# Kernel optimization log

Measured on AMD Instinct MI355X. Metric: run time of the kernel, lower is better.

Reference implementation:

```python
import jax, jax.numpy as jnp
import numpy as np

D_MODEL = 1024
N_HEADS = 16
D_HEAD = 64


def setup_inputs() -> dict:
    key = jax.random.key(0)
    kx, kq, kk, kv, ko = jax.random.split(key, 5)
    B, T = 2, 2048
    inner = N_HEADS * D_HEAD
    s = 1.0 / np.sqrt(D_MODEL)
    return {
        "x": jax.random.normal(kx, (B, T, D_MODEL), dtype=jnp.float32),
        "Wq": jax.random.normal(kq, (D_MODEL, inner), dtype=jnp.float32) * s,
        "Wk": jax.random.normal(kk, (D_MODEL, inner), dtype=jnp.float32) * s,
        "Wv": jax.random.normal(kv, (D_MODEL, inner), dtype=jnp.float32) * s,
        "Wo": jax.random.normal(ko, (inner, D_MODEL), dtype=jnp.float32) * (1.0 / np.sqrt(inner)),
    }


def reference(x, Wq, Wk, Wv, Wo):
    B, T, D = x.shape
    H, d = N_HEADS, D_HEAD
    q = (x @ Wq).reshape(B, T, H, d)
    k = (x @ Wk).reshape(B, T, H, d)
    v = (x @ Wv).reshape(B, T, H, d)
    # scale=False -> no 1/sqrt(d) scaling
    scores = jnp.einsum('bthd,bshd->bhts', q, k)
    # strictly-lower-triangular mask (tril with diagonal=-1): s < t kept
    mask = jnp.tril(jnp.ones((T, T), dtype=bool), k=-1)
    scores = jnp.where(mask, scores, 0.0)
    out = jnp.einsum('bhts,bshd->bthd', scores, v).reshape(B, T, H * d)
    return out @ Wo
```

## Files before the change

kernel.cpp:

```cpp
#include <hip/hip_runtime.h>
#include <hip/hip_bf16.h>

#define TSEQ   2048
#define DM     1024
#define NHEAD  16
#define DH     64
#define BATCH  2
#define MR     (BATCH * TSEQ)
#define CH     64
#define NC     (TSEQ / CH)
#define QKVLD  (3 * DM)
#define LP     72

typedef __attribute__((ext_vector_type(8))) short bf16x8;
typedef __attribute__((ext_vector_type(4))) float f32x4;

__device__ __forceinline__ short f2bf(float x) {
  __hip_bfloat16 h = __float2bfloat16(x);
  return *reinterpret_cast<short*>(&h);
}

__device__ __forceinline__ void stage16(const void* g, void* l) {
  __builtin_amdgcn_global_load_lds(
      (const __attribute__((address_space(1))) void*)g,
      (__attribute__((address_space(3))) void*)l, 16, 0, 0);
}

__global__ __launch_bounds__(256) void gemm_qkv(const short* __restrict__ A,
                                                const short* __restrict__ Bt,
                                                short* __restrict__ qb,
                                                short* __restrict__ kb,
                                                short* __restrict__ kT,
                                                short* __restrict__ vT) {
  const int K = DM;
  __shared__ short As[2][128][32];
  __shared__ short Bs[2][128][32];
  const int tid = threadIdx.x;
  const int lane = tid & 63, wid = tid >> 6;
  const int wave_m = wid >> 1, wave_n = wid & 1;
  const int row0 = blockIdx.y * 128, col0 = blockIdx.x * 128;

  const int sr = tid >> 2, sk = (tid & 3) * 8;
  const short* Ag0 = A + (size_t)(row0 + sr) * K + sk;
  const short* Bg0 = Bt + (size_t)(col0 + sr) * K + sk;
  short* AsL = &As[0][0][0] + tid * 8;
  short* BsL = &Bs[0][0][0] + tid * 8;

  f32x4 acc[4][4];
#pragma unroll
  for (int i = 0; i < 4; ++i)
#pragma unroll
    for (int j = 0; j < 4; ++j) acc[i][j] = (f32x4){0.f, 0.f, 0.f, 0.f};

  const int fm = wave_m * 64 + (lane & 15);
  const int fn = wave_n * 64 + (lane & 15);
  const int fk = (lane >> 4) * 8;

  for (int k0 = 0; k0 < K; k0 += 64) {
    stage16(Ag0 + k0, AsL);
    stage16(Ag0 + (size_t)64 * K + k0, AsL + 2048);
    stage16(Ag0 + k0 + 32, AsL + 4096);
    stage16(Ag0 + (size_t)64 * K + k0 + 32, AsL + 6144);
    stage16(Bg0 + k0, BsL);
    stage16(Bg0 + (size_t)64 * K + k0, BsL + 2048);
    stage16(Bg0 + k0 + 32, BsL + 4096);
    stage16(Bg0 + (size_t)64 * K + k0 + 32, BsL + 6144);
    __syncthreads();
#pragma unroll
    for (int p = 0; p < 2; ++p) {
      bf16x8 af[4], bf[4];
#pragma unroll
      for (int t = 0; t < 4; ++t) {
        af[t] = *(const bf16x8*)&As[p][fm + t * 16][fk];
        bf[t] = *(const bf16x8*)&Bs[p][fn + t * 16][fk];
      }
#pragma unroll
      for (int im = 0; im < 4; ++im)
#pragma unroll
        for (int jn = 0; jn < 4; ++jn)
          acc[im][jn] = __builtin_amdgcn_mfma_f32_16x16x32_bf16(af[im], bf[jn], acc[im][jn], 0, 0, 0);
    }
    __syncthreads();
  }

  const int crow = (lane >> 4) * 4, ccol = lane & 15;
  const int region = col0 >> 10;

  if (region <= 1) {
    short* Cb = (region == 0) ? qb : kb;
#pragma unroll
    for (int im = 0; im < 4; ++im)
#pragma unroll
      for (int jn = 0; jn < 4; ++jn) {
        const int gr = row0 + wave_m * 64 + im * 16 + crow;
        const int gc = (col0 & 1023) + wave_n * 64 + jn * 16 + ccol;
        short* Cp = Cb + (size_t)gr * DM + gc;
#pragma unroll
        for (int r = 0; r < 4; ++r) Cp[(size_t)r * DM] = f2bf(acc[im][jn][r]);
      }
  }
  if (region >= 1) {
    short* Tt = (region == 1) ? kT : vT;
    const int gr0 = row0 + wave_m * 64;
    const int b = gr0 >> 11;
    const int c = (gr0 & 2047) >> 6;
#pragma unroll
    for (int im = 0; im < 4; ++im)
#pragma unroll
      for (int jn = 0; jn < 4; ++jn) {
        const int gcol = (col0 & 1023) + wave_n * 64 + jn * 16 + ccol;
        const int h = gcol >> 6, i = gcol & 63;
        const int s0 = im * 16 + crow;
        size_t idx = ((((size_t)(b * NHEAD + h) * NC + c) * DH + i) * DH + s0);
        union { short h4[4]; uint2 u; } pk;
#pragma unroll
        for (int r = 0; r < 4; ++r) pk.h4[r] = f2bf(acc[im][jn][r]);
        *(uint2*)(Tt + idx) = pk.u;
      }
  }
}

__global__ __launch_bounds__(256) void gemm_out(const short* __restrict__ A,
                                                const short* __restrict__ Bt,
                                                float* __restrict__ C) {
  const int K = DM, N = DM;
  __shared__ short As[128][32];
  __shared__ short Bs[64][32];
  const int tid = threadIdx.x, lane = tid & 63, wid = tid >> 6;
  const int row0 = blockIdx.y * 128, col0 = blockIdx.x * 64;

  const int sr = tid >> 2, sk = (tid & 3) * 8;
  const short* Ag0 = A + (size_t)(row0 + sr) * K + sk;
  const short* Bg0 = Bt + (size_t)(col0 + sr) * K + sk;
  short* AsL = &As[0][0] + tid * 8;
  short* BsL = &Bs[0][0] + tid * 8;

  f32x4 acc[2][4];
#pragma unroll
  for (int i = 0; i < 2; ++i)
#pragma unroll
    for (int j = 0; j < 4; ++j) acc[i][j] = (f32x4){0.f, 0.f, 0.f, 0.f};

  const int fm = wid * 32 + (lane & 15);
  const int fn = lane & 15;
  const int fk = (lane >> 4) * 8;

  for (int k0 = 0; k0 < K; k0 += 32) {
    stage16(Ag0 + k0, AsL);
    stage16(Ag0 + (size_t)64 * K + k0, AsL + 2048);
    stage16(Bg0 + k0, BsL);
    __syncthreads();
    bf16x8 af[2], bf[4];
#pragma unroll
    for (int t = 0; t < 2; ++t) af[t] = *(const bf16x8*)&As[fm + t * 16][fk];
#pragma unroll
    for (int t = 0; t < 4; ++t) bf[t] = *(const bf16x8*)&Bs[t * 16 + fn][fk];
#pragma unroll
    for (int im = 0; im < 2; ++im)
#pragma unroll
      for (int jn = 0; jn < 4; ++jn)
        acc[im][jn] = __builtin_amdgcn_mfma_f32_16x16x32_bf16(af[im], bf[jn], acc[im][jn], 0, 0, 0);
    __syncthreads();
  }

  const int crow = (lane >> 4) * 4, ccol = lane & 15;
#pragma unroll
  for (int im = 0; im < 2; ++im)
#pragma unroll
    for (int jn = 0; jn < 4; ++jn) {
      float* Cp = C + (size_t)(row0 + wid * 32 + im * 16 + crow) * N
                    + col0 + jn * 16 + ccol;
#pragma unroll
      for (int r = 0; r < 4; ++r) Cp[(size_t)r * N] = acc[im][jn][r];
    }
}

__global__ __launch_bounds__(256) void prep(const float* __restrict__ x,
                                            const float* __restrict__ W0,
                                            const float* __restrict__ W1,
                                            const float* __restrict__ W2,
                                            const float* __restrict__ W3,
                                            __hip_bfloat16* __restrict__ xb,
                                            __hip_bfloat16* __restrict__ Wt) {
  const int tid = threadIdx.x;
  if (blockIdx.z == 4) {
    const int bid = blockIdx.y * 16 + blockIdx.x;
    const float* src = x + (size_t)bid * 16384;
    __hip_bfloat16* dst = xb + (size_t)bid * 16384;
#pragma unroll
    for (int it = 0; it < 16; ++it) {
      int i = it * 1024 + tid * 4;
      float4 v = *(const float4*)(src + i);
      union { __hip_bfloat16 h[4]; uint2 u; } pk;
      pk.h[0] = __float2bfloat16(v.x); pk.h[1] = __float2bfloat16(v.y);
      pk.h[2] = __float2bfloat16(v.z); pk.h[3] = __float2bfloat16(v.w);
      *(uint2*)(dst + i) = pk.u;
    }
    return;
  }
  const float* W = blockIdx.z == 0 ? W0 : blockIdx.z == 1 ? W1 : blockIdx.z == 2 ? W2 : W3;
  __hip_bfloat16* out = Wt + (size_t)blockIdx.z * DM * DM;
  __shared__ float tile[64][65];
  const int kt = blockIdx.y * 64, nt = blockIdx.x * 64;
  const int lr = tid >> 6, lc = tid & 63;
#pragma unroll
  for (int i = 0; i < 16; ++i) {
    int k = i * 4 + lr;
    tile[k][lc] = W[(size_t)(kt + k) * DM + nt + lc];
  }
  __syncthreads();
  const int nl = tid >> 4, k4 = (tid & 15) * 4;
#pragma unroll
  for (int i = 0; i < 4; ++i) {
    int n = i * 16 + nl;
    union { __hip_bfloat16 h[4]; uint2 u; } pk;
#pragma unroll
    for (int xx = 0; xx < 4; ++xx) pk.h[xx] = __float2bfloat16(tile[k4 + xx][n]);
    *(uint2*)(out + (size_t)(nt + n) * DM + kt + k4) = pk.u;
  }
}

__global__ __launch_bounds__(256) void state_scan(const short* __restrict__ kT,
                                                  const short* __restrict__ vT,
                                                  short* __restrict__ Spre) {
  const int js = blockIdx.x, h = blockIdx.y, b = blockIdx.z;
  const int tid = threadIdx.x, lane = tid & 63, w = tid >> 6;
  const int m = lane & 15, q = lane >> 4;
  const size_t hbase = ((size_t)(b * NHEAD + h) * NC) * (DH * DH);
  const int jrow = 16 * js + m;
  const int irow = 16 * w + m;
  f32x4 run = (f32x4){0.f, 0.f, 0.f, 0.f};
  for (int c = 0; c < NC; ++c) {
    const size_t tile = hbase + (size_t)c * (DH * DH);
#pragma unroll
    for (int rr = 0; rr < 4; ++rr)
      Spre[tile + (size_t)(16 * js + q * 4 + rr) * DH + 16 * w + m] = f2bf(run[rr]);
    bf16x8 a0 = *(const bf16x8*)(vT + tile + (size_t)jrow * DH + q * 8);
    bf16x8 a1 = *(const bf16x8*)(vT + tile + (size_t)jrow * DH + q * 8 + 32);
    bf16x8 b0 = *(const bf16x8*)(kT + tile + (size_t)irow * DH + q * 8);
    bf16x8 b1 = *(const bf16x8*)(kT + tile + (size_t)irow * DH + q * 8 + 32);
    f32x4 t = (f32x4){0.f, 0.f, 0.f, 0.f};
    t = __builtin_amdgcn_mfma_f32_16x16x32_bf16(a0, b0, t, 0, 0, 0);
    t = __builtin_amdgcn_mfma_f32_16x16x32_bf16(a1, b1, t, 0, 0, 0);
    run += t;
  }
}

__global__ __launch_bounds__(256) void intra_attn(const short* __restrict__ qb,
                                                  const short* __restrict__ kb,
                                                  const short* __restrict__ vT,
                                                  const short* __restrict__ Spre,
                                                  short* __restrict__ O_) {
  const int c = blockIdx.x, h = blockIdx.y, b = blockIdx.z;
  __shared__ short Qs[CH][LP];
  __shared__ short Ks[CH][LP];
  const int tid = threadIdx.x, lane = tid & 63, w = tid >> 6;
  const int m = lane & 15, q = lane >> 4;
  const int r = tid >> 2, q16 = (tid & 3) * 16;
  const size_t tile = ((size_t)(b * NHEAD + h) * NC + c) * (DH * DH);
  const size_t grow = ((size_t)(b * TSEQ + c * CH + r)) * DM + h * DH;
  *(bf16x8*)&Qs[r][q16]     = *(const bf16x8*)(qb + grow + q16);
  *(bf16x8*)&Qs[r][q16 + 8] = *(const bf16x8*)(qb + grow + q16 + 8);
  *(bf16x8*)&Ks[r][q16]     = *(const bf16x8*)(kb + grow + q16);
  *(bf16x8*)&Ks[r][q16 + 8] = *(const bf16x8*)(kb + grow + q16 + 8);
  const short* vt = vT + tile;
  const short* st = Spre + tile;
  bf16x8 av0 = *(const bf16x8*)(vt + (16 * w + m) * DH + q * 8);
  bf16x8 av1 = *(const bf16x8*)(vt + (16 * w + m) * DH + q * 8 + 32);
  bf16x8 as0 = *(const bf16x8*)(st + (16 * w + m) * DH + q * 8);
  bf16x8 as1 = *(const bf16x8*)(st + (16 * w + m) * DH + q * 8 + 32);
  __syncthreads();

  bf16x8 aq0 = *(const bf16x8*)&Qs[16 * w + m][q * 8];
  bf16x8 aq1 = *(const bf16x8*)&Qs[16 * w + m][q * 8 + 32];

  f32x4 acc[4], pacc[4];
#pragma unroll
  for (int ct = 0; ct < 4; ++ct) {
    acc[ct] = (f32x4){0.f, 0.f, 0.f, 0.f};
    pacc[ct] = (f32x4){0.f, 0.f, 0.f, 0.f};
  }
#pragma unroll
  for (int ct = 0; ct < 4; ++ct) {
    bf16x8 bq0 = *(const bf16x8*)&Qs[ct * 16 + m][q * 8];
    bf16x8 bq1 = *(const bf16x8*)&Qs[ct * 16 + m][q * 8 + 32];
    acc[ct] = __builtin_amdgcn_mfma_f32_16x16x32_bf16(as0, bq0, acc[ct], 0, 0, 0);
    acc[ct] = __builtin_amdgcn_mfma_f32_16x16x32_bf16(as1, bq1, acc[ct], 0, 0, 0);
    bf16x8 bk0 = *(const bf16x8*)&Ks[ct * 16 + m][q * 8];
    bf16x8 bk1 = *(const bf16x8*)&Ks[ct * 16 + m][q * 8 + 32];
    pacc[ct] = __builtin_amdgcn_mfma_f32_16x16x32_bf16(aq0, bk0, pacc[ct], 0, 0, 0);
    pacc[ct] = __builtin_amdgcn_mfma_f32_16x16x32_bf16(aq1, bk1, pacc[ct], 0, 0, 0);
  }
  __syncthreads();
#pragma unroll
  for (int ct = 0; ct < 4; ++ct) {
    const int s = ct * 16 + m;
#pragma unroll
    for (int rr = 0; rr < 4; ++rr) {
      const int t = 16 * w + q * 4 + rr;
      Ks[t][s] = f2bf((s < t) ? pacc[ct][rr] : 0.f);
    }
  }
  __syncthreads();
#pragma unroll
  for (int ct = 0; ct < 4; ++ct) {
    bf16x8 bp0 = *(const bf16x8*)&Ks[ct * 16 + m][q * 8];
    bf16x8 bp1 = *(const bf16x8*)&Ks[ct * 16 + m][q * 8 + 32];
    acc[ct] = __builtin_amdgcn_mfma_f32_16x16x32_bf16(av0, bp0, acc[ct], 0, 0, 0);
    acc[ct] = __builtin_amdgcn_mfma_f32_16x16x32_bf16(av1, bp1, acc[ct], 0, 0, 0);
  }
#pragma unroll
  for (int ct = 0; ct < 4; ++ct) {
    const int t = ct * 16 + m, j0 = 16 * w + q * 4;
    union { short h4[4]; uint2 u; } pk;
#pragma unroll
    for (int rr = 0; rr < 4; ++rr) pk.h4[rr] = f2bf(acc[ct][rr]);
    *(uint2*)(O_ + ((size_t)(b * TSEQ + c * CH + t)) * DM + h * DH + j0) = pk.u;
  }
}

extern "C" void kernel_launch(void* const* d_in, const int* in_sizes, int n_in,
                              void* d_out, int out_size, void* d_ws, size_t ws_size,
                              hipStream_t stream) {
  const float* x  = (const float*)d_in[0];
  const float* Wq = (const float*)d_in[1];
  const float* Wk = (const float*)d_in[2];
  const float* Wv = (const float*)d_in[3];
  const float* Wo = (const float*)d_in[4];
  float* out = (float*)d_out;

  char* ws = (char*)d_ws;
  short* xb    = (short*)ws;  ws += (size_t)MR * DM * 2;
  short* WtAll = (short*)ws;  ws += (size_t)4 * DM * DM * 2;
  short* qb    = (short*)ws;  ws += (size_t)MR * DM * 2;
  short* kb    = (short*)ws;  ws += (size_t)MR * DM * 2;
  short* kT    = (short*)ws;  ws += (size_t)MR * DM * 2;
  short* vT    = (short*)ws;  ws += (size_t)MR * DM * 2;
  short* Spre  = (short*)ws;  ws += (size_t)MR * DM * 2;
  short* aob   = (short*)ws;  ws += (size_t)MR * DM * 2;

  prep<<<dim3(16, 16, 5), 256, 0, stream>>>(x, Wq, Wk, Wv, Wo,
                                            (__hip_bfloat16*)xb, (__hip_bfloat16*)WtAll);

  gemm_qkv<<<dim3(QKVLD / 128, MR / 128), 256, 0, stream>>>(xb, WtAll, qb, kb, kT, vT);

  state_scan<<<dim3(4, NHEAD, BATCH), 256, 0, stream>>>(kT, vT, Spre);

  intra_attn<<<dim3(NC, NHEAD, BATCH), 256, 0, stream>>>(qb, kb, vT, Spre, aob);

  gemm_out<<<dim3(DM / 64, MR / 128), 256, 0, stream>>>(
      aob, WtAll + (size_t)3 * DM * DM, out);
}
```

Before: 174.3 us.

## Fuse all stages into one cooperative persistent kernel with grid syncs

Merges the prep, QKV GEMM, state scan, intra-chunk attention and output GEMM stages into a single cooperative persistent kernel. Stages are separated by grid.sync and the grid is sized from occupancy. The aim is to remove per-launch overhead and tail gaps between the five kernels. The QKV GEMM also drops from a 64-wide K step to a 32-wide step so its shared-memory footprint fits the common buffer, which doubles its barrier count. Grid-wide barriers, low parallelism in the 128-unit scan stage, and launch_bounds(256,2) register limits may offset the gains; a fallback path launches separate kernels.

```diff
diff --git a/kernel.cpp b/kernel.cpp
--- a/kernel.cpp
+++ b/kernel.cpp
@@ -1,5 +1,8 @@
 #include <hip/hip_runtime.h>
 #include <hip/hip_bf16.h>
+#include <hip/hip_cooperative_groups.h>
+
+namespace cg = cooperative_groups;
 
 #define TSEQ   2048
 #define DM     1024
@@ -11,6 +14,7 @@
 #define NC     (TSEQ / CH)
 #define QKVLD  (3 * DM)
 #define LP     72
+#define SMEMB  18432
 
 typedef __attribute__((ext_vector_type(8))) short bf16x8;
 typedef __attribute__((ext_vector_type(4))) float f32x4;
@@ -26,25 +30,68 @@
       (__attribute__((address_space(3))) void*)l, 16, 0, 0);
 }
 
-__global__ __launch_bounds__(256) void gemm_qkv(const short* __restrict__ A,
-                                                const short* __restrict__ Bt,
-                                                short* __restrict__ qb,
-                                                short* __restrict__ kb,
-                                                short* __restrict__ kT,
-                                                short* __restrict__ vT) {
+
+__device__ __forceinline__ void dev_prep_unit(
+    int u, const float* __restrict__ x, const float* __restrict__ Wq,
+    const float* __restrict__ Wk, const float* __restrict__ Wv,
+    const float* __restrict__ Wo, short* __restrict__ xb,
+    short* __restrict__ WtAll, char* smem) {
+  const int tid = threadIdx.x;
+  __syncthreads();
+  const int z = u >> 8, wv = u & 255;
+  if (z == 4) {
+    const float* src = x + (size_t)wv * 16384;
+    short* dst = xb + (size_t)wv * 16384;
+#pragma unroll
+    for (int it = 0; it < 16; ++it) {
+      int i = it * 1024 + tid * 4;
+      float4 v = *(const float4*)(src + i);
+      union { short h[4]; uint2 uu; } pk;
+      pk.h[0] = f2bf(v.x); pk.h[1] = f2bf(v.y);
+      pk.h[2] = f2bf(v.z); pk.h[3] = f2bf(v.w);
+      *(uint2*)(dst + i) = pk.uu;
+    }
+  } else {
+    const int bx = wv & 15, by = wv >> 4;
+    const float* W = z == 0 ? Wq : z == 1 ? Wk : z == 2 ? Wv : Wo;
+    short* o = WtAll + (size_t)z * DM * DM;
+    float (*tile)[65] = (float(*)[65])smem;
+    const int kt = by * 64, nt = bx * 64;
+    const int lr = tid >> 6, lc = tid & 63;
+#pragma unroll
+    for (int i = 0; i < 16; ++i) {
+      int k = i * 4 + lr;
+      tile[k][lc] = W[(size_t)(kt + k) * DM + nt + lc];
+    }
+    __syncthreads();
+    const int nl = tid >> 4, k4 = (tid & 15) * 4;
+#pragma unroll
+    for (int i = 0; i < 4; ++i) {
+      int n = i * 16 + nl;
+      union { short h[4]; uint2 uu; } pk;
+#pragma unroll
+      for (int xx = 0; xx < 4; ++xx) pk.h[xx] = f2bf(tile[k4 + xx][n]);
+      *(uint2*)(o + (size_t)(nt + n) * DM + kt + k4) = pk.uu;
+    }
+  }
+}
+
+__device__ __forceinline__ void dev_qkv_tile(
+    int bx, int by, const short* __restrict__ A, const short* __restrict__ Bt,
+    short* __restrict__ qb, short* __restrict__ kb,
+    short* __restrict__ kT, short* __restrict__ vT, char* smem) {
   const int K = DM;
-  __shared__ short As[2][128][32];
-  __shared__ short Bs[2][128][32];
-  const int tid = threadIdx.x;
-  const int lane = tid & 63, wid = tid >> 6;
+  short (*As)[32] = (short(*)[32])smem;
+  short (*Bs)[32] = (short(*)[32])(smem + 8192);
+  const int tid = threadIdx.x, lane = tid & 63, wid = tid >> 6;
   const int wave_m = wid >> 1, wave_n = wid & 1;
-  const int row0 = blockIdx.y * 128, col0 = blockIdx.x * 128;
+  const int row0 = by * 128, col0 = bx * 128;
 
   const int sr = tid >> 2, sk = (tid & 3) * 8;
   const short* Ag0 = A + (size_t)(row0 + sr) * K + sk;
   const short* Bg0 = Bt + (size_t)(col0 + sr) * K + sk;
-  short* AsL = &As[0][0][0] + tid * 8;
-  short* BsL = &Bs[0][0][0] + tid * 8;
+  short* AsL = &As[0][0] + tid * 8;
+  short* BsL = &Bs[0][0] + tid * 8;
 
   f32x4 acc[4][4];
 #pragma unroll
@@ -56,30 +103,24 @@
   const int fn = wave_n * 64 + (lane & 15);
   const int fk = (lane >> 4) * 8;
 
-  for (int k0 = 0; k0 < K; k0 += 64) {
+  __syncthreads();
+  for (int k0 = 0; k0 < K; k0 += 32) {
     stage16(Ag0 + k0, AsL);
     stage16(Ag0 + (size_t)64 * K + k0, AsL + 2048);
-    stage16(Ag0 + k0 + 32, AsL + 4096);
-    stage16(Ag0 + (size_t)64 * K + k0 + 32, AsL + 6144);
     stage16(Bg0 + k0, BsL);
     stage16(Bg0 + (size_t)64 * K + k0, BsL + 2048);
-    stage16(Bg0 + k0 + 32, BsL + 4096);
-    stage16(Bg0 + (size_t)64 * K + k0 + 32, BsL + 6144);
     __syncthreads();
-#pragma unroll
-    for (int p = 0; p < 2; ++p) {
-      bf16x8 af[4], bf[4];
-#pragma unroll
-      for (int t = 0; t < 4; ++t) {
-        af[t] = *(const bf16x8*)&As[p][fm + t * 16][fk];
-        bf[t] = *(const bf16x8*)&Bs[p][fn + t * 16][fk];
-      }
-#pragma unroll
-      for (int im = 0; im < 4; ++im)
-#pragma unroll
-        for (int jn = 0; jn < 4; ++jn)
-          acc[im][jn] = __builtin_amdgcn_mfma_f32_16x16x32_bf16(af[im], bf[jn], acc[im][jn], 0, 0, 0);
-    }
+    bf16x8 af[4], bf[4];
+#pragma unroll
+    for (int t = 0; t < 4; ++t) {
+      af[t] = *(const bf16x8*)&As[fm + t * 16][fk];
+      bf[t] = *(const bf16x8*)&Bs[fn + t * 16][fk];
+    }
+#pragma unroll
+    for (int im = 0; im < 4; ++im)
+#pragma unroll
+      for (int jn = 0; jn < 4; ++jn)
+        acc[im][jn] = __builtin_amdgcn_mfma_f32_16x16x32_bf16(af[im], bf[jn], acc[im][jn], 0, 0, 0);
     __syncthreads();
   }
 
@@ -112,118 +153,18 @@
         const int h = gcol >> 6, i = gcol & 63;
         const int s0 = im * 16 + crow;
         size_t idx = ((((size_t)(b * NHEAD + h) * NC + c) * DH + i) * DH + s0);
-        union { short h4[4]; uint2 u; } pk;
+        union { short h4[4]; uint2 uu; } pk;
 #pragma unroll
         for (int r = 0; r < 4; ++r) pk.h4[r] = f2bf(acc[im][jn][r]);
-        *(uint2*)(Tt + idx) = pk.u;
+        *(uint2*)(Tt + idx) = pk.uu;
       }
   }
 }
 
-__global__ __launch_bounds__(256) void gemm_out(const short* __restrict__ A,
-                                                const short* __restrict__ Bt,
-                                                float* __restrict__ C) {
-  const int K = DM, N = DM;
-  __shared__ short As[128][32];
-  __shared__ short Bs[64][32];
-  const int tid = threadIdx.x, lane = tid & 63, wid = tid >> 6;
-  const int row0 = blockIdx.y * 128, col0 = blockIdx.x * 64;
-
-  const int sr = tid >> 2, sk = (tid & 3) * 8;
-  const short* Ag0 = A + (size_t)(row0 + sr) * K + sk;
-  const short* Bg0 = Bt + (size_t)(col0 + sr) * K + sk;
-  short* AsL = &As[0][0] + tid * 8;
-  short* BsL = &Bs[0][0] + tid * 8;
-
-  f32x4 acc[2][4];
-#pragma unroll
-  for (int i = 0; i < 2; ++i)
-#pragma unroll
-    for (int j = 0; j < 4; ++j) acc[i][j] = (f32x4){0.f, 0.f, 0.f, 0.f};
-
-  const int fm = wid * 32 + (lane & 15);
-  const int fn = lane & 15;
-  const int fk = (lane >> 4) * 8;
-
-  for (int k0 = 0; k0 < K; k0 += 32) {
-    stage16(Ag0 + k0, AsL);
-    stage16(Ag0 + (size_t)64 * K + k0, AsL + 2048);
-    stage16(Bg0 + k0, BsL);
-    __syncthreads();
-    bf16x8 af[2], bf[4];
-#pragma unroll
-    for (int t = 0; t < 2; ++t) af[t] = *(const bf16x8*)&As[fm + t * 16][fk];
-#pragma unroll
-    for (int t = 0; t < 4; ++t) bf[t] = *(const bf16x8*)&Bs[t * 16 + fn][fk];
-#pragma unroll
-    for (int im = 0; im < 2; ++im)
-#pragma unroll
-      for (int jn = 0; jn < 4; ++jn)
-        acc[im][jn] = __builtin_amdgcn_mfma_f32_16x16x32_bf16(af[im], bf[jn], acc[im][jn], 0, 0, 0);
-    __syncthreads();
-  }
-
-  const int crow = (lane >> 4) * 4, ccol = lane & 15;
-#pragma unroll
-  for (int im = 0; im < 2; ++im)
-#pragma unroll
-    for (int jn = 0; jn < 4; ++jn) {
-      float* Cp = C + (size_t)(row0 + wid * 32 + im * 16 + crow) * N
-                    + col0 + jn * 16 + ccol;
-#pragma unroll
-      for (int r = 0; r < 4; ++r) Cp[(size_t)r * N] = acc[im][jn][r];
-    }
-}
-
-__global__ __launch_bounds__(256) void prep(const float* __restrict__ x,
-                                            const float* __restrict__ W0,
-                                            const float* __restrict__ W1,
-                                            const float* __restrict__ W2,
-                                            const float* __restrict__ W3,
-                                            __hip_bfloat16* __restrict__ xb,
-                                            __hip_bfloat16* __restrict__ Wt) {
-  const int tid = threadIdx.x;
-  if (blockIdx.z == 4) {
-    const int bid = blockIdx.y * 16 + blockIdx.x;
-    const float* src = x + (size_t)bid * 16384;
-    __hip_bfloat16* dst = xb + (size_t)bid * 16384;
-#pragma unroll
-    for (int it = 0; it < 16; ++it) {
-      int i = it * 1024 + tid * 4;
-      float4 v = *(const float4*)(src + i);
-      union { __hip_bfloat16 h[4]; uint2 u; } pk;
-      pk.h[0] = __float2bfloat16(v.x); pk.h[1] = __float2bfloat16(v.y);
-      pk.h[2] = __float2bfloat16(v.z); pk.h[3] = __float2bfloat16(v.w);
-      *(uint2*)(dst + i) = pk.u;
-    }
-    return;
-  }
-  const float* W = blockIdx.z == 0 ? W0 : blockIdx.z == 1 ? W1 : blockIdx.z == 2 ? W2 : W3;
-  __hip_bfloat16* out = Wt + (size_t)blockIdx.z * DM * DM;
-  __shared__ float tile[64][65];
-  const int kt = blockIdx.y * 64, nt = blockIdx.x * 64;
-  const int lr = tid >> 6, lc = tid & 63;
-#pragma unroll
-  for (int i = 0; i < 16; ++i) {
-    int k = i * 4 + lr;
-    tile[k][lc] = W[(size_t)(kt + k) * DM + nt + lc];
-  }
-  __syncthreads();
-  const int nl = tid >> 4, k4 = (tid & 15) * 4;
-#pragma unroll
-  for (int i = 0; i < 4; ++i) {
-    int n = i * 16 + nl;
-    union { __hip_bfloat16 h[4]; uint2 u; } pk;
-#pragma unroll
-    for (int xx = 0; xx < 4; ++xx) pk.h[xx] = __float2bfloat16(tile[k4 + xx][n]);
-    *(uint2*)(out + (size_t)(nt + n) * DM + kt + k4) = pk.u;
-  }
-}
-
-__global__ __launch_bounds__(256) void state_scan(const short* __restrict__ kT,
-                                                  const short* __restrict__ vT,
-                                                  short* __restrict__ Spre) {
-  const int js = blockIdx.x, h = blockIdx.y, b = blockIdx.z;
+__device__ __forceinline__ void dev_state_unit(
+    int u, const short* __restrict__ kT, const short* __restrict__ vT,
+    short* __restrict__ Spre) {
+  const int js = u & 3, h = (u >> 2) & 15, b = u >> 6;
   const int tid = threadIdx.x, lane = tid & 63, w = tid >> 6;
   const int m = lane & 15, q = lane >> 4;
   const size_t hbase = ((size_t)(b * NHEAD + h) * NC) * (DH * DH);
@@ -246,19 +187,19 @@
   }
 }
 
-__global__ __launch_bounds__(256) void intra_attn(const short* __restrict__ qb,
-                                                  const short* __restrict__ kb,
-                                                  const short* __restrict__ vT,
-                                                  const short* __restrict__ Spre,
-                                                  short* __restrict__ O_) {
-  const int c = blockIdx.x, h = blockIdx.y, b = blockIdx.z;
-  __shared__ short Qs[CH][LP];
-  __shared__ short Ks[CH][LP];
+__device__ __forceinline__ void dev_intra_unit(
+    int u, const short* __restrict__ qb, const short* __restrict__ kb,
+    const short* __restrict__ vT, const short* __restrict__ Spre,
+    short* __restrict__ aob, char* smem) {
+  const int c = u & 31, h = (u >> 5) & 15, b = u >> 9;
+  short (*Qs)[LP] = (short(*)[LP])smem;
+  short (*Ks)[LP] = (short(*)[LP])(smem + 9216);
   const int tid = threadIdx.x, lane = tid & 63, w = tid >> 6;
   const int m = lane & 15, q = lane >> 4;
   const int r = tid >> 2, q16 = (tid & 3) * 16;
   const size_t tile = ((size_t)(b * NHEAD + h) * NC + c) * (DH * DH);
   const size_t grow = ((size_t)(b * TSEQ + c * CH + r)) * DM + h * DH;
+  __syncthreads();
   *(bf16x8*)&Qs[r][q16]     = *(const bf16x8*)(qb + grow + q16);
   *(bf16x8*)&Qs[r][q16 + 8] = *(const bf16x8*)(qb + grow + q16 + 8);
   *(bf16x8*)&Ks[r][q16]     = *(const bf16x8*)(kb + grow + q16);
@@ -312,11 +253,126 @@
 #pragma unroll
   for (int ct = 0; ct < 4; ++ct) {
     const int t = ct * 16 + m, j0 = 16 * w + q * 4;
-    union { short h4[4]; uint2 u; } pk;
+    union { short h4[4]; uint2 uu; } pk;
 #pragma unroll
     for (int rr = 0; rr < 4; ++rr) pk.h4[rr] = f2bf(acc[ct][rr]);
-    *(uint2*)(O_ + ((size_t)(b * TSEQ + c * CH + t)) * DM + h * DH + j0) = pk.u;
-  }
+    *(uint2*)(aob + ((size_t)(b * TSEQ + c * CH + t)) * DM + h * DH + j0) = pk.uu;
+  }
+}
+
+__device__ __forceinline__ void dev_out_tile(
+    int bx, int by, const short* __restrict__ A, const short* __restrict__ Bt,
+    float* __restrict__ C, char* smem) {
+  const int K = DM, N = DM;
+  short (*As)[32] = (short(*)[32])smem;
+  short (*Bs)[32] = (short(*)[32])(smem + 8192);
+  const int tid = threadIdx.x, lane = tid & 63, wid = tid >> 6;
+  const int row0 = by * 128, col0 = bx * 64;
+
+  const int sr = tid >> 2, sk = (tid & 3) * 8;
+  const short* Ag0 = A + (size_t)(row0 + sr) * K + sk;
+  const short* Bg0 = Bt + (size_t)(col0 + sr) * K + sk;
+  short* AsL = &As[0][0] + tid * 8;
+  short* BsL = &Bs[0][0] + tid * 8;
+
+  f32x4 acc[2][4];
+#pragma unroll
+  for (int i = 0; i < 2; ++i)
+#pragma unroll
+    for (int j = 0; j < 4; ++j) acc[i][j] = (f32x4){0.f, 0.f, 0.f, 0.f};
+
+  const int fm = wid * 32 + (lane & 15);
+  const int fn = lane & 15;
+  const int fk = (lane >> 4) * 8;
+
+  for (int k0 = 0; k0 < K; k0 += 32) {
+    __syncthreads();
+    stage16(Ag0 + k0, AsL);
+    stage16(Ag0 + (size_t)64 * K + k0, AsL + 2048);
+    stage16(Bg0 + k0, BsL);
+    __syncthreads();
+    bf16x8 af[2], bf[4];
+#pragma unroll
+    for (int t = 0; t < 2; ++t) af[t] = *(const bf16x8*)&As[fm + t * 16][fk];
+#pragma unroll
+    for (int t = 0; t < 4; ++t) bf[t] = *(const bf16x8*)&Bs[t * 16 + fn][fk];
+#pragma unroll
+    for (int im = 0; im < 2; ++im)
+#pragma unroll
+      for (int jn = 0; jn < 4; ++jn)
+        acc[im][jn] = __builtin_amdgcn_mfma_f32_16x16x32_bf16(af[im], bf[jn], acc[im][jn], 0, 0, 0);
+  }
+
+  const int crow = (lane >> 4) * 4, ccol = lane & 15;
+#pragma unroll
+  for (int im = 0; im < 2; ++im)
+#pragma unroll
+    for (int jn = 0; jn < 4; ++jn) {
+      float* Cp = C + (size_t)(row0 + wid * 32 + im * 16 + crow) * N
+                    + col0 + jn * 16 + ccol;
+#pragma unroll
+      for (int r = 0; r < 4; ++r) Cp[(size_t)r * N] = acc[im][jn][r];
+    }
+}
+
+__global__ __launch_bounds__(256, 2) void fused_all(
+    const float* __restrict__ x,  const float* __restrict__ Wq,
+    const float* __restrict__ Wk, const float* __restrict__ Wv,
+    const float* __restrict__ Wo, float* __restrict__ out,
+    short* __restrict__ xb,   short* __restrict__ WtAll,
+    short* __restrict__ qb,   short* __restrict__ kb,
+    short* __restrict__ kT,   short* __restrict__ vT,
+    short* __restrict__ Spre, short* __restrict__ aob) {
+  cg::grid_group grid = cg::this_grid();
+  __shared__ __align__(16) char smem[SMEMB];
+  const int bid = blockIdx.x, gsz = gridDim.x;
+
+  for (int u = bid; u < 1280; u += gsz)
+    dev_prep_unit(u, x, Wq, Wk, Wv, Wo, xb, WtAll, smem);
+  __threadfence();
+  grid.sync();
+
+  for (int u = bid; u < 768; u += gsz)
+    dev_qkv_tile(u % 24, u / 24, xb, WtAll, qb, kb, kT, vT, smem);
+  __threadfence();
+  grid.sync();
+
+  for (int u = bid; u < 128; u += gsz)
+    dev_state_unit(u, kT, vT, Spre);
+  __threadfence();
+  grid.sync();
+
+  for (int u = bid; u < 1024; u += gsz)
+    dev_intra_unit(u, qb, kb, vT, Spre, aob, smem);
+  __threadfence();
+  grid.sync();
+
+  for (int u = bid; u < 512; u += gsz)
+    dev_out_tile(u & 15, u >> 4, aob, WtAll + (size_t)3 * DM * DM, out, smem);
+}
+
+__global__ __launch_bounds__(256) void k_prep(const float* x, const float* Wq,
+                                              const float* Wk, const float* Wv,
+                                              const float* Wo, short* xb, short* WtAll) {
+  __shared__ __align__(16) char smem[SMEMB];
+  dev_prep_unit(blockIdx.x, x, Wq, Wk, Wv, Wo, xb, WtAll, smem);
+}
+__global__ __launch_bounds__(256) void k_qkv(const short* xb, const short* WtAll,
+                                             short* qb, short* kb, short* kT, short* vT) {
+  __shared__ __align__(16) char smem[SMEMB];
+  dev_qkv_tile(blockIdx.x % 24, blockIdx.x / 24, xb, WtAll, qb, kb, kT, vT, smem);
+}
+__global__ __launch_bounds__(256) void k_scan(const short* kT, const short* vT, short* Spre) {
+  dev_state_unit(blockIdx.x, kT, vT, Spre);
+}
+__global__ __launch_bounds__(256) void k_intra(const short* qb, const short* kb,
+                                               const short* vT, const short* Spre, short* aob) {
+  __shared__ __align__(16) char smem[SMEMB];
+  dev_intra_unit(blockIdx.x, qb, kb, vT, Spre, aob, smem);
+}
+__global__ __launch_bounds__(256) void k_out(const short* aob, const short* WoT, float* out) {
+  __shared__ __align__(16) char smem[SMEMB];
+  dev_out_tile(blockIdx.x & 15, blockIdx.x >> 4, aob, WoT, out, smem);
 }
 
 extern "C" void kernel_launch(void* const* d_in, const int* in_sizes, int n_in,
@@ -338,16 +394,28 @@
   short* vT    = (short*)ws;  ws += (size_t)MR * DM * 2;
   short* Spre  = (short*)ws;  ws += (size_t)MR * DM * 2;
   short* aob   = (short*)ws;  ws += (size_t)MR * DM * 2;
-
-  prep<<<dim3(16, 16, 5), 256, 0, stream>>>(x, Wq, Wk, Wv, Wo,
-                                            (__hip_bfloat16*)xb, (__hip_bfloat16*)WtAll);
-
-  gemm_qkv<<<dim3(QKVLD / 128, MR / 128), 256, 0, stream>>>(xb, WtAll, qb, kb, kT, vT);
-
-  state_scan<<<dim3(4, NHEAD, BATCH), 256, 0, stream>>>(kT, vT, Spre);
-
-  intra_attn<<<dim3(NC, NHEAD, BATCH), 256, 0, stream>>>(qb, kb, vT, Spre, aob);
-
-  gemm_out<<<dim3(DM / 64, MR / 128), 256, 0, stream>>>(
-      aob, WtAll + (size_t)3 * DM * DM, out);
-}
+  short* WoT   = WtAll + (size_t)3 * DM * DM;
+
+  int occ = 0;
+  hipError_t eq = hipOccupancyMaxActiveBlocksPerMultiprocessor(
+      &occ, (const void*)fused_all, 256, 0);
+  bool coop_ok = (eq == hipSuccess) && (occ >= 2);
+
+  if (coop_ok) {
+    int nblk = occ * 256;
+    if (nblk > 768) nblk = 768;
+    void* kargs[] = {(void*)&x,  (void*)&Wq,  (void*)&Wk,   (void*)&Wv,
+                     (void*)&Wo, (void*)&out, (void*)&xb,   (void*)&WtAll,
+                     (void*)&qb, (void*)&kb,  (void*)&kT,   (void*)&vT,
+                     (void*)&Spre, (void*)&aob};
+    hipError_t el = hipLaunchCooperativeKernel((void*)fused_all, dim3(nblk),
+                                               dim3(256), kargs, 0, stream);
+    if (el == hipSuccess) return;
+  }
+
+  k_prep<<<1280, 256, 0, stream>>>(x, Wq, Wk, Wv, Wo, xb, WtAll);
+  k_qkv<<<768, 256, 0, stream>>>(xb, WtAll, qb, kb, kT, vT);
+  k_scan<<<128, 256, 0, stream>>>(kT, vT, Spre);
+  k_intra<<<1024, 256, 0, stream>>>(qb, kb, vT, Spre, aob);
+  k_out<<<512, 256, 0, stream>>>(aob, WoT, out);
+}
```

After: 648.9 us. 272% more time.
